# Performance work log

Hardware: AMD Instinct MI355X
Metric: run time of the kernel (lower is better)

## Reference

```python
import jax, jax.numpy as jnp
import numpy as np

BS, M, D, H = 64, 2048, 1024, 1024  # batch, memory_num, embed dim, attention hidden


def setup_inputs() -> dict:
    key = jax.random.key(0)
    ks = jax.random.split(key, 6)
    s = 1.0 / np.sqrt(D)
    return {
        "query": jax.random.normal(ks[0], (BS, D), dtype=jnp.float32),
        "memory": jax.random.normal(ks[1], (BS, M, D), dtype=jnp.float32),
        "Wq": jax.random.normal(ks[2], (H, D), dtype=jnp.float32) * s,
        "bq": jax.random.normal(ks[3], (H,), dtype=jnp.float32) * s,
        "Wm": jax.random.normal(ks[4], (H, D), dtype=jnp.float32) * s,
        "v": jax.random.normal(ks[5], (H,), dtype=jnp.float32) * s,
    }


def reference(query, memory, Wq, bq, Wm, v):
    # perceptual (additive) attention:
    # hidden = tanh(Wq q + bq + Wm m)  -> [bs, M, H]
    q_proj = query @ Wq.T + bq                       # [bs, H]
    m_proj = jnp.einsum('bmd,hd->bmh', memory, Wm)   # [bs, M, H]
    hidden = jnp.tanh(q_proj[:, None, :] + m_proj)   # [bs, M, H]
    attn = jnp.einsum('bmh,h->bm', hidden, v)        # [bs, M]
    weights = jax.nn.softmax(attn, axis=-1)[:, None, :]          # [bs, 1, M]
    weighted_memory = jnp.einsum('bqm,bmd->bqd', weights, memory)  # [bs, 1, D]
    return weights, weighted_memory
```

## Files before the change

### kernel.cpp

```cpp
#include <hip/hip_runtime.h>
#include <stdint.h>
#include <stddef.h>

#define BSZ 64
#define MM  2048
#define DD  1024
#define HH  1024
#define RR  (BSZ * MM)

typedef float  float4v  __attribute__((ext_vector_type(4)));
typedef float  float8v  __attribute__((ext_vector_type(8)));
typedef short  short4v  __attribute__((ext_vector_type(4)));
typedef short  short8v  __attribute__((ext_vector_type(8)));
typedef __bf16 bf16x4v  __attribute__((ext_vector_type(4)));
typedef __bf16 bf16x8v  __attribute__((ext_vector_type(8)));

__device__ __forceinline__ short8v cvt_f32x8_bf16(float4v lo, float4v hi) {
    float8v f;
    f[0] = lo[0]; f[1] = lo[1]; f[2] = lo[2]; f[3] = lo[3];
    f[4] = hi[0]; f[5] = hi[1]; f[6] = hi[2]; f[7] = hi[3];
    union { bf16x8v b; short8v s; } u;
    u.b = __builtin_convertvector(f, bf16x8v);
    return u.s;
}

__device__ __forceinline__ float fast_tanh(float x) {
    float ax = __builtin_fabsf(x);
    float e  = __builtin_amdgcn_exp2f(ax * -2.88539008177792681f);
    float r  = __builtin_amdgcn_rcpf(1.0f + e);
    float t  = __builtin_fmaf(-2.0f * e, r, 1.0f);
    return __builtin_copysignf(t, x);
}

__global__ __launch_bounds__(256) void cast_wm_kernel(const float* __restrict__ wm,
                                                      short* __restrict__ out) {
    int i = (blockIdx.x * 256 + threadIdx.x) * 4;
    float4v f = *(const float4v*)(wm + i);
    union { bf16x4v b; short4v s; } u;
    u.b = __builtin_convertvector(f, bf16x4v);
    *(short4v*)(out + i) = u.s;
}

__global__ __launch_bounds__(256) void qproj_kernel(const float* __restrict__ query,
                                                    const float* __restrict__ Wq,
                                                    const float* __restrict__ bq,
                                                    float* __restrict__ qproj) {
    __shared__ __align__(16) float qs[DD];
    const int b = blockIdx.y;
    const int h = blockIdx.x * 256 + threadIdx.x;
    for (int i = threadIdx.x; i < DD; i += 256) qs[i] = query[b * DD + i];
    __syncthreads();
    const float4v* wrow = (const float4v*)(Wq + (size_t)h * DD);
    float acc = 0.0f;
#pragma unroll 4
    for (int d4 = 0; d4 < DD / 4; ++d4) {
        float4v w = wrow[d4];
        float4v q = *(const float4v*)(qs + d4 * 4);
        acc += w[0] * q[0] + w[1] * q[1] + w[2] * q[2] + w[3] * q[3];
    }
    qproj[b * HH + h] = acc + bq[h];
}

__global__ __launch_bounds__(256) void gemm_attn_kernel(
    const float* __restrict__ memf, const short* __restrict__ wmbf,
    const float* __restrict__ qproj, const float* __restrict__ vvec,
    float* __restrict__ attn) {
    __shared__ __align__(16) float As[128 * 32];
    __shared__ __align__(16) short Bs[128 * 32];

    const int tid  = threadIdx.x;
    const int lane = tid & 63;
    const int wave = tid >> 6;
    const int wx = wave & 1, wy = wave >> 1;

    const int bi    = blockIdx.x;
    const int xcd   = bi & 7;
    const int idx   = bi >> 3;
    const int tileR = xcd * 128 + (idx >> 3);
    const int tileC = idx & 7;
    const int r0 = tileR * 128;
    const int h0 = tileC * 128;

    const float* aptr[4];
#pragma unroll
    for (int j = 0; j < 4; ++j) {
        int i   = wave * 4 + j;
        int row = i * 8 + (lane >> 3);
        int col = ((lane & 7) ^ (lane >> 3)) * 4;
        aptr[j] = memf + (size_t)(r0 + row) * DD + col;
    }
    const short* bptr[2];
#pragma unroll
    for (int j = 0; j < 2; ++j) {
        int i   = wave * 2 + j;
        int row = i * 16 + (lane >> 2);
        int col = ((lane & 3) ^ ((lane >> 3) & 3)) * 8;
        bptr[j] = wmbf + (size_t)(h0 + row) * DD + col;
    }

    float4v acc[4][4];
#pragma unroll
    for (int a = 0; a < 4; ++a)
#pragma unroll
        for (int b = 0; b < 4; ++b) acc[a][b] = (float4v)0.0f;

    const int c  = lane & 15;
    const int g  = lane >> 4;

    for (int kt = 0; kt < DD / 32; ++kt) {
        __syncthreads();
#pragma unroll
        for (int j = 0; j < 4; ++j) {
            __builtin_amdgcn_global_load_lds(
                (const __attribute__((address_space(1))) void*)(aptr[j]),
                (__attribute__((address_space(3))) void*)((char*)As + (wave * 4 + j) * 1024),
                16, 0, 0);
            aptr[j] += 32;
        }
#pragma unroll
        for (int j = 0; j < 2; ++j) {
            __builtin_amdgcn_global_load_lds(
                (const __attribute__((address_space(1))) void*)(bptr[j]),
                (__attribute__((address_space(3))) void*)((char*)Bs + (wave * 2 + j) * 1024),
                16, 0, 0);
            bptr[j] += 32;
        }
        __syncthreads();

        short8v bfr[4];
#pragma unroll
        for (int nf = 0; nf < 4; ++nf) {
            int n  = wx * 64 + nf * 16 + c;
            int gb = g ^ ((n >> 1) & 3);
            bfr[nf] = *(const short8v*)(Bs + n * 32 + gb * 8);
        }
#pragma unroll
        for (int mf = 0; mf < 4; ++mf) {
            int m  = wy * 64 + mf * 16 + c;
            int sw = m & 7;
            int gl = (g * 2) ^ sw;
            int gh = (g * 2 + 1) ^ sw;
            float4v lo = *(const float4v*)(As + m * 32 + gl * 4);
            float4v hi = *(const float4v*)(As + m * 32 + gh * 4);
            short8v afr = cvt_f32x8_bf16(lo, hi);
#pragma unroll
            for (int nf = 0; nf < 4; ++nf)
                acc[mf][nf] = __builtin_amdgcn_mfma_f32_16x16x32_bf16(
                    afr, bfr[nf], acc[mf][nf], 0, 0, 0);
        }
    }

    const int b = tileR >> 4;
    float vv[4], qp[4];
#pragma unroll
    for (int nf = 0; nf < 4; ++nf) {
        int h   = h0 + wx * 64 + nf * 16 + c;
        vv[nf] = vvec[h];
        qp[nf] = qproj[b * HH + h];
    }
    float rs[4][4];
#pragma unroll
    for (int mf = 0; mf < 4; ++mf)
#pragma unroll
        for (int r = 0; r < 4; ++r) rs[mf][r] = 0.0f;
#pragma unroll
    for (int mf = 0; mf < 4; ++mf)
#pragma unroll
        for (int nf = 0; nf < 4; ++nf)
#pragma unroll
            for (int r = 0; r < 4; ++r)
                rs[mf][r] += fast_tanh(acc[mf][nf][r] + qp[nf]) * vv[nf];

#pragma unroll
    for (int mf = 0; mf < 4; ++mf)
#pragma unroll
        for (int r = 0; r < 4; ++r) {
            float s = rs[mf][r];
            s += __shfl_xor(s, 1);
            s += __shfl_xor(s, 2);
            s += __shfl_xor(s, 4);
            s += __shfl_xor(s, 8);
            if (c == 0)
                atomicAdd(attn + (r0 + wy * 64 + mf * 16 + g * 4 + r), s);
        }
}

__global__ __launch_bounds__(256) void softmax_kernel(const float* __restrict__ attn,
                                                      float* __restrict__ wout) {
    const int b = blockIdx.x, tid = threadIdx.x;
    __shared__ float red[8];
    float a[8];
    float mx = -1e30f;
#pragma unroll
    for (int i = 0; i < 8; ++i) {
        a[i] = attn[b * MM + i * 256 + tid];
        mx = fmaxf(mx, a[i]);
    }
#pragma unroll
    for (int off = 1; off < 64; off <<= 1) mx = fmaxf(mx, __shfl_xor(mx, off));
    if ((tid & 63) == 0) red[tid >> 6] = mx;
    __syncthreads();
    mx = fmaxf(fmaxf(red[0], red[1]), fmaxf(red[2], red[3]));
    float s = 0.0f;
#pragma unroll
    for (int i = 0; i < 8; ++i) {
        a[i] = __builtin_amdgcn_exp2f((a[i] - mx) * 1.4426950408889634f);
        s += a[i];
    }
#pragma unroll
    for (int off = 1; off < 64; off <<= 1) s += __shfl_xor(s, off);
    if ((tid & 63) == 0) red[4 + (tid >> 6)] = s;
    __syncthreads();
    s = red[4] + red[5] + red[6] + red[7];
    float inv = 1.0f / s;
#pragma unroll
    for (int i = 0; i < 8; ++i) wout[b * MM + i * 256 + tid] = a[i] * inv;
}

__global__ __launch_bounds__(256) void wmem_kernel(const float* __restrict__ mem,
                                                   const float* __restrict__ w,
                                                   float* __restrict__ out2) {
    const int b  = blockIdx.z;
    const int d  = blockIdx.x * 256 + threadIdx.x;
    const int m0 = blockIdx.y * 512;
    __shared__ float wsh[512];
    for (int i = threadIdx.x; i < 512; i += 256) wsh[i] = w[b * MM + m0 + i];
    __syncthreads();
    const float* mp = mem + ((size_t)(b * MM + m0)) * DD + d;
    float acc = 0.0f;
#pragma unroll 8
    for (int m = 0; m < 512; ++m)
        acc = __builtin_fmaf(wsh[m], mp[(size_t)m * DD], acc);
    atomicAdd(out2 + b * DD + d, acc);
}

extern "C" void kernel_launch(void* const* d_in, const int* in_sizes, int n_in,
                              void* d_out, int out_size, void* d_ws, size_t ws_size,
                              hipStream_t stream) {
    const float* query  = (const float*)d_in[0];
    const float* memory = (const float*)d_in[1];
    const float* Wq     = (const float*)d_in[2];
    const float* bq     = (const float*)d_in[3];
    const float* Wm     = (const float*)d_in[4];
    const float* v      = (const float*)d_in[5];

    float* out      = (float*)d_out;
    float* wout     = out;
    float* wmem_out = out + BSZ * MM;

    char*  ws    = (char*)d_ws;
    float* qproj = (float*)ws;
    float* attn  = (float*)(ws + 262144);
    short* wmbf  = (short*)(ws + 786432);

    hipMemsetAsync(attn, 0, (size_t)RR * sizeof(float), stream);
    hipMemsetAsync(d_out, 0, (size_t)out_size * sizeof(float), stream);

    cast_wm_kernel<<<HH * DD / (256 * 4), 256, 0, stream>>>(Wm, wmbf);
    qproj_kernel<<<dim3(HH / 256, BSZ), 256, 0, stream>>>(query, Wq, bq, qproj);
    gemm_attn_kernel<<<(RR / 128) * (HH / 128), 256, 0, stream>>>(memory, wmbf, qproj, v, attn);
    softmax_kernel<<<BSZ, 256, 0, stream>>>(attn, wout);
    wmem_kernel<<<dim3(DD / 256, 4, BSZ), 256, 0, stream>>>(memory, wout, wmem_out);
}
```

Baseline: 1.181 ms.

## Enlarge GEMM tiles to 256x256 with double-buffered LDS prefetch and vectorize wmem

```diff
diff --git a/kernel.cpp b/kernel.cpp
--- a/kernel.cpp
+++ b/kernel.cpp
@@ -14,6 +14,9 @@
 typedef short  short8v  __attribute__((ext_vector_type(8)));
 typedef __bf16 bf16x4v  __attribute__((ext_vector_type(4)));
 typedef __bf16 bf16x8v  __attribute__((ext_vector_type(8)));
+
+#define AS1 __attribute__((address_space(1)))
+#define AS3 __attribute__((address_space(3)))
 
 __device__ __forceinline__ short8v cvt_f32x8_bf16(float4v lo, float4v hi) {
     float8v f;
@@ -61,127 +64,174 @@
     qproj[b * HH + h] = acc + bq[h];
 }
 
-__global__ __launch_bounds__(256) void gemm_attn_kernel(
+__global__ __launch_bounds__(512, 2) void gemm_attn_kernel(
     const float* __restrict__ memf, const short* __restrict__ wmbf,
     const float* __restrict__ qproj, const float* __restrict__ vvec,
     float* __restrict__ attn) {
-    __shared__ __align__(16) float As[128 * 32];
-    __shared__ __align__(16) short Bs[128 * 32];
+    extern __shared__ __align__(16) char smem[];
+    float* As = (float*)smem;
+    short* Bs = (short*)(smem + 65536);
 
     const int tid  = threadIdx.x;
     const int lane = tid & 63;
     const int wave = tid >> 6;
-    const int wx = wave & 1, wy = wave >> 1;
+    const int wm   = wave >> 1;
+    const int wn   = wave & 1;
 
     const int bi    = blockIdx.x;
-    const int xcd   = bi & 7;
-    const int idx   = bi >> 3;
-    const int tileR = xcd * 128 + (idx >> 3);
-    const int tileC = idx & 7;
-    const int r0 = tileR * 128;
-    const int h0 = tileC * 128;
+    const int wg    = (bi & 7) * 256 + (bi >> 3);
+    const int tileR = wg >> 2;
+    const int tileC = wg & 3;
+    const int r0 = tileR * 256;
+    const int h0 = tileC * 256;
 
     const float* aptr[4];
 #pragma unroll
     for (int j = 0; j < 4; ++j) {
-        int i   = wave * 4 + j;
-        int row = i * 8 + (lane >> 3);
+        int row = (wave * 4 + j) * 8 + (lane >> 3);
         int col = ((lane & 7) ^ (lane >> 3)) * 4;
         aptr[j] = memf + (size_t)(r0 + row) * DD + col;
     }
     const short* bptr[2];
 #pragma unroll
     for (int j = 0; j < 2; ++j) {
-        int i   = wave * 2 + j;
-        int row = i * 16 + (lane >> 2);
+        int row = (wave * 2 + j) * 16 + (lane >> 2);
         int col = ((lane & 3) ^ ((lane >> 3) & 3)) * 8;
         bptr[j] = wmbf + (size_t)(h0 + row) * DD + col;
     }
 
-    float4v acc[4][4];
-#pragma unroll
-    for (int a = 0; a < 4; ++a)
-#pragma unroll
-        for (int b = 0; b < 4; ++b) acc[a][b] = (float4v)0.0f;
-
-    const int c  = lane & 15;
-    const int g  = lane >> 4;
-
-    for (int kt = 0; kt < DD / 32; ++kt) {
-        __syncthreads();
-#pragma unroll
-        for (int j = 0; j < 4; ++j) {
-            __builtin_amdgcn_global_load_lds(
-                (const __attribute__((address_space(1))) void*)(aptr[j]),
-                (__attribute__((address_space(3))) void*)((char*)As + (wave * 4 + j) * 1024),
-                16, 0, 0);
-            aptr[j] += 32;
+    const int c = lane & 15;
+    const int g = lane >> 4;
+
+    int offAlo[4], offAhi[4];
+#pragma unroll
+    for (int mf = 0; mf < 4; ++mf) {
+        int m  = wm * 64 + mf * 16 + c;
+        int sw = m & 7;
+        offAlo[mf] = m * 32 + ((g * 2) ^ sw) * 4;
+        offAhi[mf] = m * 32 + ((g * 2 + 1) ^ sw) * 4;
+    }
+    int offB[8];
+#pragma unroll
+    for (int nf = 0; nf < 8; ++nf) {
+        int n = wn * 128 + nf * 16 + c;
+        offB[nf] = n * 32 + (g ^ ((n >> 1) & 3)) * 8;
+    }
+
+    float4v acc[4][8];
+#pragma unroll
+    for (int mf = 0; mf < 4; ++mf)
+#pragma unroll
+        for (int nf = 0; nf < 8; ++nf) acc[mf][nf] = (float4v)0.0f;
+
+#pragma unroll
+    for (int j = 0; j < 4; ++j) {
+        __builtin_amdgcn_global_load_lds(
+            (const AS1 void*)aptr[j],
+            (AS3 void*)(smem + (wave * 4 + j) * 1024), 16, 0, 0);
+        aptr[j] += 32;
+    }
+#pragma unroll
+    for (int j = 0; j < 2; ++j) {
+        __builtin_amdgcn_global_load_lds(
+            (const AS1 void*)bptr[j],
+            (AS3 void*)(smem + 65536 + (wave * 2 + j) * 1024), 16, 0, 0);
+        bptr[j] += 32;
+    }
+    asm volatile("s_waitcnt vmcnt(0)" ::: "memory");
+    asm volatile("s_barrier" ::: "memory");
+
+    short8v afr[4], bfr[2];
+
+    for (int t = 0; t < 32; ++t) {
+        const int cur = t & 1;
+        const int nxt = cur ^ 1;
+        const float* Ab = As + cur * 8192;
+        const short* Bb = Bs + cur * 8192;
+        char* AnB = smem + nxt * 32768;
+        char* BnB = smem + 65536 + nxt * 16384;
+        const bool pf = (t < 31);
+
+#pragma unroll
+        for (int p = 0; p < 4; ++p) {
+            float4v alo[4], ahi[4];
+            if (p == 0) {
+#pragma unroll
+                for (int mf = 0; mf < 4; ++mf) {
+                    alo[mf] = *(const float4v*)(Ab + offAlo[mf]);
+                    ahi[mf] = *(const float4v*)(Ab + offAhi[mf]);
+                }
+            }
+            bfr[0] = *(const short8v*)(Bb + offB[2 * p]);
+            bfr[1] = *(const short8v*)(Bb + offB[2 * p + 1]);
+
+            if (p == 0 && pf) {
+                __builtin_amdgcn_global_load_lds((const AS1 void*)aptr[0],
+                    (AS3 void*)(AnB + (wave * 4 + 0) * 1024), 16, 0, 0);
+                __builtin_amdgcn_global_load_lds((const AS1 void*)aptr[1],
+                    (AS3 void*)(AnB + (wave * 4 + 1) * 1024), 16, 0, 0);
+                aptr[0] += 32; aptr[1] += 32;
+            } else if (p == 1 && pf) {
+                __builtin_amdgcn_global_load_lds((const AS1 void*)aptr[2],
+                    (AS3 void*)(AnB + (wave * 4 + 2) * 1024), 16, 0, 0);
+                __builtin_amdgcn_global_load_lds((const AS1 void*)aptr[3],
+                    (AS3 void*)(AnB + (wave * 4 + 3) * 1024), 16, 0, 0);
+                aptr[2] += 32; aptr[3] += 32;
+            } else if (p == 2 && pf) {
+                __builtin_amdgcn_global_load_lds((const AS1 void*)bptr[0],
+                    (AS3 void*)(BnB + (wave * 2 + 0) * 1024), 16, 0, 0);
+                __builtin_amdgcn_global_load_lds((const AS1 void*)bptr[1],
+                    (AS3 void*)(BnB + (wave * 2 + 1) * 1024), 16, 0, 0);
+                bptr[0] += 32; bptr[1] += 32;
+            }
+
+            asm volatile("s_barrier" ::: "memory");
+            asm volatile("s_waitcnt lgkmcnt(0)" ::: "memory");
+            __builtin_amdgcn_sched_barrier(0);
+
+            if (p == 0) {
+#pragma unroll
+                for (int mf = 0; mf < 4; ++mf)
+                    afr[mf] = cvt_f32x8_bf16(alo[mf], ahi[mf]);
+            }
+
+            __builtin_amdgcn_s_setprio(1);
+#pragma unroll
+            for (int mf = 0; mf < 4; ++mf) {
+                acc[mf][2 * p] = __builtin_amdgcn_mfma_f32_16x16x32_bf16(
+                    afr[mf], bfr[0], acc[mf][2 * p], 0, 0, 0);
+                acc[mf][2 * p + 1] = __builtin_amdgcn_mfma_f32_16x16x32_bf16(
+                    afr[mf], bfr[1], acc[mf][2 * p + 1], 0, 0, 0);
+            }
+            __builtin_amdgcn_s_setprio(0);
+
+            if (p == 3) asm volatile("s_waitcnt vmcnt(0)" ::: "memory");
+            asm volatile("s_barrier" ::: "memory");
         }
-#pragma unroll
-        for (int j = 0; j < 2; ++j) {
-            __builtin_amdgcn_global_load_lds(
-                (const __attribute__((address_space(1))) void*)(bptr[j]),
-                (__attribute__((address_space(3))) void*)((char*)Bs + (wave * 2 + j) * 1024),
-                16, 0, 0);
-            bptr[j] += 32;
-        }
-        __syncthreads();
-
-        short8v bfr[4];
-#pragma unroll
-        for (int nf = 0; nf < 4; ++nf) {
-            int n  = wx * 64 + nf * 16 + c;
-            int gb = g ^ ((n >> 1) & 3);
-            bfr[nf] = *(const short8v*)(Bs + n * 32 + gb * 8);
-        }
-#pragma unroll
-        for (int mf = 0; mf < 4; ++mf) {
-            int m  = wy * 64 + mf * 16 + c;
-            int sw = m & 7;
-            int gl = (g * 2) ^ sw;
-            int gh = (g * 2 + 1) ^ sw;
-            float4v lo = *(const float4v*)(As + m * 32 + gl * 4);
-            float4v hi = *(const float4v*)(As + m * 32 + gh * 4);
-            short8v afr = cvt_f32x8_bf16(lo, hi);
-#pragma unroll
-            for (int nf = 0; nf < 4; ++nf)
-                acc[mf][nf] = __builtin_amdgcn_mfma_f32_16x16x32_bf16(
-                    afr, bfr[nf], acc[mf][nf], 0, 0, 0);
-        }
-    }
-
-    const int b = tileR >> 4;
-    float vv[4], qp[4];
-#pragma unroll
-    for (int nf = 0; nf < 4; ++nf) {
-        int h   = h0 + wx * 64 + nf * 16 + c;
+    }
+
+    const int b = tileR >> 3;
+    float vv[8], qp[8];
+#pragma unroll
+    for (int nf = 0; nf < 8; ++nf) {
+        int h  = h0 + wn * 128 + nf * 16 + c;
         vv[nf] = vvec[h];
         qp[nf] = qproj[b * HH + h];
     }
-    float rs[4][4];
 #pragma unroll
     for (int mf = 0; mf < 4; ++mf)
 #pragma unroll
-        for (int r = 0; r < 4; ++r) rs[mf][r] = 0.0f;
-#pragma unroll
-    for (int mf = 0; mf < 4; ++mf)
-#pragma unroll
-        for (int nf = 0; nf < 4; ++nf)
-#pragma unroll
-            for (int r = 0; r < 4; ++r)
-                rs[mf][r] += fast_tanh(acc[mf][nf][r] + qp[nf]) * vv[nf];
-
-#pragma unroll
-    for (int mf = 0; mf < 4; ++mf)
-#pragma unroll
         for (int r = 0; r < 4; ++r) {
-            float s = rs[mf][r];
+            float s = 0.0f;
+#pragma unroll
+            for (int nf = 0; nf < 8; ++nf)
+                s += fast_tanh(acc[mf][nf][r] + qp[nf]) * vv[nf];
             s += __shfl_xor(s, 1);
             s += __shfl_xor(s, 2);
             s += __shfl_xor(s, 4);
             s += __shfl_xor(s, 8);
             if (c == 0)
-                atomicAdd(attn + (r0 + wy * 64 + mf * 16 + g * 4 + r), s);
+                atomicAdd(attn + (r0 + wm * 64 + mf * 16 + g * 4 + r), s);
         }
 }
 
@@ -220,18 +270,28 @@
 __global__ __launch_bounds__(256) void wmem_kernel(const float* __restrict__ mem,
                                                    const float* __restrict__ w,
                                                    float* __restrict__ out2) {
-    const int b  = blockIdx.z;
-    const int d  = blockIdx.x * 256 + threadIdx.x;
-    const int m0 = blockIdx.y * 512;
-    __shared__ float wsh[512];
-    for (int i = threadIdx.x; i < 512; i += 256) wsh[i] = w[b * MM + m0 + i];
+    const int m0 = blockIdx.x * 256;
+    const int b  = blockIdx.y;
+    __shared__ float wsh[256];
+    wsh[threadIdx.x] = w[b * MM + m0 + threadIdx.x];
     __syncthreads();
-    const float* mp = mem + ((size_t)(b * MM + m0)) * DD + d;
-    float acc = 0.0f;
+    const float4v* mp = (const float4v*)(mem + ((size_t)(b * MM + m0)) * DD)
+                        + threadIdx.x;
+    float4v acc = (float4v)0.0f;
 #pragma unroll 8
-    for (int m = 0; m < 512; ++m)
-        acc = __builtin_fmaf(wsh[m], mp[(size_t)m * DD], acc);
-    atomicAdd(out2 + b * DD + d, acc);
+    for (int m = 0; m < 256; ++m) {
+        float wv = wsh[m];
+        float4v x = mp[(size_t)m * 256];
+        acc[0] = __builtin_fmaf(wv, x[0], acc[0]);
+        acc[1] = __builtin_fmaf(wv, x[1], acc[1]);
+        acc[2] = __builtin_fmaf(wv, x[2], acc[2]);
+        acc[3] = __builtin_fmaf(wv, x[3], acc[3]);
+    }
+    float* o = out2 + b * DD + threadIdx.x * 4;
+    atomicAdd(o + 0, acc[0]);
+    atomicAdd(o + 1, acc[1]);
+    atomicAdd(o + 2, acc[2]);
+    atomicAdd(o + 3, acc[3]);
 }
 
 extern "C" void kernel_launch(void* const* d_in, const int* in_sizes, int n_in,
@@ -253,12 +313,19 @@
     float* attn  = (float*)(ws + 262144);
     short* wmbf  = (short*)(ws + 786432);
 
+    static bool attr_done = false;
+    if (!attr_done) {
+        hipFuncSetAttribute((const void*)gemm_attn_kernel,
+                            hipFuncAttributeMaxDynamicSharedMemorySize, 98304);
+        attr_done = true;
+    }
+
     hipMemsetAsync(attn, 0, (size_t)RR * sizeof(float), stream);
     hipMemsetAsync(d_out, 0, (size_t)out_size * sizeof(float), stream);
 
     cast_wm_kernel<<<HH * DD / (256 * 4), 256, 0, stream>>>(Wm, wmbf);
     qproj_kernel<<<dim3(HH / 256, BSZ), 256, 0, stream>>>(query, Wq, bq, qproj);
-    gemm_attn_kernel<<<(RR / 128) * (HH / 128), 256, 0, stream>>>(memory, wmbf, qproj, v, attn);
+    gemm_attn_kernel<<<(RR / 256) * (HH / 256), 512, 98304, stream>>>(memory, wmbf, qproj, v, attn);
     softmax_kernel<<<BSZ, 256, 0, stream>>>(attn, wout);
-    wmem_kernel<<<dim3(DD / 256, 4, BSZ), 256, 0, stream>>>(memory, wout, wmem_out);
-}
+    wmem_kernel<<<dim3(MM / 256, BSZ), 256, 0, stream>>>(memory, wout, wmem_out);
+}
```

Result: faster. 1.122 ms (-5.0%).
